# Performance work log

Hardware: AMD Instinct MI355X
Metric: run time of the kernel (lower is better)

The kernel has to match this reference:

```python
import jax, jax.numpy as jnp
import numpy as np

B, C, O = 16, 32, 32
IH, IW = 64, 64
KH, KW = 3, 3
PH, PW = 1, 1
SH, SW = 1, 1
OH = (IH + 2 * PH - KH) // SH + 1  # 64
OW = (IW + 2 * PW - KW) // SW + 1  # 64


def setup_inputs() -> dict:
    key = jax.random.key(0)
    kx, kw = jax.random.split(key)
    x = jax.random.normal(kx, (B, C, IH, IW), dtype=jnp.float32)
    # per-output-location (non-shared) weights: (O, C, OH, OW, KH*KW)
    weight = jax.random.normal(kw, (O, C, OH, OW, KH * KW), dtype=jnp.float32)
    return {"x": x, "weight": weight}


def _patches(x):
    # pad=1 on both spatial dims, then extract KHxKW patches with stride 1
    xp = jnp.pad(x, ((0, 0), (0, 0), (PH, PH), (PW, PW)))
    # ordering matches torch unfold(2,kh).unfold(3,kw) -> flatten last two dims
    pats = [xp[:, :, i : i + OH * SH : SH, j : j + OW * SW : SW]
            for i in range(KH) for j in range(KW)]
    return jnp.stack(pats, axis=-1)  # [B, C, OH, OW, KH*KW]


def reference(x, weight):
    p = _patches(x)  # [B, C, OH, OW, K]
    # fused broadcast-mul + sum over (C, K): per-pixel independent contraction
    out = jnp.einsum('bchwk,ochwk->bohw', p, weight)
    return out  # [B, O, OH, OW]
```

## Files before the change

kernel.cpp:

```cpp
#include <hip/hip_runtime.h>
#include <hip/hip_bf16.h>


#define CIN  32
#define OCH  32
#define HH   64
#define WW   64
#define BB   8
#define OO   2
#define CC   16

typedef float f32x4 __attribute__((ext_vector_type(4), aligned(4)));

__device__ __forceinline__ float lane_pick(int byte_addr, float v) {
    return __int_as_float(__builtin_amdgcn_ds_bpermute(byte_addr, __float_as_int(v)));
}

__global__ __launch_bounds__(256)
void lc2d_kernel(const float* __restrict__ x,
                 const float* __restrict__ wt,
                 float* __restrict__ out) {
    const int w  = threadIdx.x;
    const int h  = blockIdx.x * 4 + threadIdx.y;
    const int og = blockIdx.y;
    const int bz = blockIdx.z & 1;
    const int cg = blockIdx.z >> 1;
    const int o0 = og * OO;
    const int b0 = bz * BB;
    const int c0 = cg * CC;

    const float mt = (h > 0)      ? 1.f : 0.f;
    const float mb = (h < HH - 1) ? 1.f : 0.f;
    const float ml = (w > 0)      ? 1.f : 0.f;
    const float mr = (w < WW - 1) ? 1.f : 0.f;
    const int iht = (h > 0)      ? h - 1 : 0;
    const int ihb = (h < HH - 1) ? h + 1 : HH - 1;

    const int lup = ((w > 0)  ? w - 1 : 0)  << 2;
    const int ldn = ((w < 63) ? w + 1 : 63) << 2;

    float acc[OO * BB];
#pragma unroll
    for (int i = 0; i < OO * BB; ++i) acc[i] = 0.f;

    const size_t WSTRC = (size_t)HH * WW * 9;
    const size_t WSTRO = (size_t)CIN * WSTRC;
    const float* wpa = wt + (size_t)o0 * WSTRO + (size_t)c0 * WSTRC
                          + ((size_t)h * WW + w) * 9;
    const float* wpb = wpa + WSTRO;

    const float* xb0 = x + ((size_t)b0 * CIN + c0) * (HH * WW);
    const int ro_t = iht * WW + w;
    const int ro_m = h   * WW + w;
    const int ro_b = ihb * WW + w;

    f32x4 a03 = *(const f32x4*)(wpa);
    f32x4 a47 = *(const f32x4*)(wpa + 4);
    float a8  = wpa[8];
    f32x4 b03 = *(const f32x4*)(wpb);
    f32x4 b47 = *(const f32x4*)(wpb + 4);
    float b8  = wpb[8];

    for (int c = 0; c < CC; ++c) {
        const float wa0 = a03.x * (mt * ml), wa1 = a03.y * mt, wa2 = a03.z * (mt * mr);
        const float wa3 = a03.w * ml,        wa4 = a47.x,      wa5 = a47.y * mr;
        const float wa6 = a47.z * (mb * ml), wa7 = a47.w * mb, wa8 = a8 * (mb * mr);
        const float wb0 = b03.x * (mt * ml), wb1 = b03.y * mt, wb2 = b03.z * (mt * mr);
        const float wb3 = b03.w * ml,        wb4 = b47.x,      wb5 = b47.y * mr;
        const float wb6 = b47.z * (mb * ml), wb7 = b47.w * mb, wb8 = b8 * (mb * mr);

        const int cn = (c + 1 < CC) ? c + 1 : c;
        const float* npa = wpa + (size_t)cn * WSTRC;
        const float* npb = wpb + (size_t)cn * WSTRC;
        a03 = *(const f32x4*)(npa);
        a47 = *(const f32x4*)(npa + 4);
        a8  = npa[8];
        b03 = *(const f32x4*)(npb);
        b47 = *(const f32x4*)(npb + 4);
        b8  = npb[8];

        const float* xc = xb0 + (size_t)c * (HH * WW);
#pragma unroll
        for (int b = 0; b < BB; ++b) {
            const float* xp = xc + (size_t)b * (CIN * HH * WW);
            const float xt = xp[ro_t];
            const float xm = xp[ro_m];
            const float xd = xp[ro_b];
            const float xtl = lane_pick(lup, xt), xtr = lane_pick(ldn, xt);
            const float xml = lane_pick(lup, xm), xmr = lane_pick(ldn, xm);
            const float xdl = lane_pick(lup, xd), xdr = lane_pick(ldn, xd);

            float a = acc[b];
            a = fmaf(xtl, wa0, a); a = fmaf(xt, wa1, a); a = fmaf(xtr, wa2, a);
            a = fmaf(xml, wa3, a); a = fmaf(xm, wa4, a); a = fmaf(xmr, wa5, a);
            a = fmaf(xdl, wa6, a); a = fmaf(xd, wa7, a); a = fmaf(xdr, wa8, a);
            acc[b] = a;

            float bq = acc[BB + b];
            bq = fmaf(xtl, wb0, bq); bq = fmaf(xt, wb1, bq); bq = fmaf(xtr, wb2, bq);
            bq = fmaf(xml, wb3, bq); bq = fmaf(xm, wb4, bq); bq = fmaf(xmr, wb5, bq);
            bq = fmaf(xdl, wb6, bq); bq = fmaf(xd, wb7, bq); bq = fmaf(xdr, wb8, bq);
            acc[BB + b] = bq;
        }
    }

#pragma unroll
    for (int b = 0; b < BB; ++b) {
#pragma unroll
        for (int oo = 0; oo < OO; ++oo) {
            atomicAdd(out + (((size_t)(b0 + b) * OCH + (o0 + oo)) * HH + h) * WW + w,
                      acc[oo * BB + b]);
        }
    }
}

extern "C" void kernel_launch(void* const* d_in, const int* in_sizes, int n_in,
                              void* d_out, int out_size, void* d_ws, size_t ws_size,
                              hipStream_t stream) {
    const float* x  = (const float*)d_in[0];
    const float* wt = (const float*)d_in[1];
    float* out = (float*)d_out;

    hipMemsetAsync(out, 0, (size_t)out_size * sizeof(float), stream);

    dim3 block(64, 4);
    dim3 grid(HH / 4, OCH / OO, 4);
    lc2d_kernel<<<grid, block, 0, stream>>>(x, wt, out);
}
```

Measured before the change: 59.20 us.

## Double-buffer input rows across channels and pipeline lane permutes ahead of FMAs

Restructures the channel loop into a two-stage software pipeline: the x rows for the next channel are loaded into a second register buffer while the current channel is computed, alongside the existing weight prefetch. The ds_bpermute neighbor fetches are issued two batches ahead of the FMAs that use them, to hide permute latency. Launch bounds now request 4 blocks per CU. The extra buffers raise register pressure, and the launch-bound hint may force spills or cut occupancy.

New measurement: 103.4 us. 74.6% more time.

```diff
diff --git a/kernel.cpp b/kernel.cpp
--- a/kernel.cpp
+++ b/kernel.cpp
@@ -16,16 +16,93 @@
     return __int_as_float(__builtin_amdgcn_ds_bpermute(byte_addr, __float_as_int(v)));
 }
 
-__global__ __launch_bounds__(256)
+#define WSTRC ((size_t)HH * WW * 9)
+#define WSTRO ((size_t)CIN * WSTRC)
+#define XB    ((size_t)CIN * HH * WW)
+
+__device__ __forceinline__ void step(
+    int c, const float* __restrict__ wpa, const float* __restrict__ wpb,
+    const float* __restrict__ xbase,
+    float (&XC)[3][BB], float (&XN)[3][BB],
+    f32x4& cA03, f32x4& cA47, float& cA8,
+    f32x4& cB03, f32x4& cB47, float& cB8,
+    f32x4& nA03, f32x4& nA47, float& nA8,
+    f32x4& nB03, f32x4& nB47, float& nB8,
+    float (&acc)[OO * BB],
+    int ro0, int ro1, int ro2, int lup, int ldn,
+    float mt, float mb, float ml, float mr,
+    float mtml, float mtmr, float mbml, float mbmr)
+{
+    const int cn = (c + 1 < CC) ? c + 1 : c;
+    const float* npa = wpa + (size_t)cn * WSTRC;
+    const float* npb = wpb + (size_t)cn * WSTRC;
+    nA03 = *(const f32x4*)(npa);
+    nA47 = *(const f32x4*)(npa + 4);
+    nA8  = npa[8];
+    nB03 = *(const f32x4*)(npb);
+    nB47 = *(const f32x4*)(npb + 4);
+    nB8  = npb[8];
+
+    const float* xnb = xbase + (size_t)cn * (HH * WW);
+#pragma unroll
+    for (int b = 0; b < BB; ++b) {
+        const float* xp = xnb + (size_t)b * XB;
+        XN[0][b] = xp[ro0]; XN[1][b] = xp[ro1]; XN[2][b] = xp[ro2];
+    }
+
+    const float wa0 = cA03.x * mtml, wa1 = cA03.y * mt, wa2 = cA03.z * mtmr;
+    const float wa3 = cA03.w * ml,   wa4 = cA47.x,      wa5 = cA47.y * mr;
+    const float wa6 = cA47.z * mbml, wa7 = cA47.w * mb, wa8 = cA8 * mbmr;
+    const float wb0 = cB03.x * mtml, wb1 = cB03.y * mt, wb2 = cB03.z * mtmr;
+    const float wb3 = cB03.w * ml,   wb4 = cB47.x,      wb5 = cB47.y * mr;
+    const float wb6 = cB47.z * mbml, wb7 = cB47.w * mb, wb8 = cB8 * mbmr;
+
+    float pr[2][6];
+#pragma unroll
+    for (int b = 0; b < 2; ++b) {
+        pr[b][0] = lane_pick(lup, XC[0][b]); pr[b][1] = lane_pick(ldn, XC[0][b]);
+        pr[b][2] = lane_pick(lup, XC[1][b]); pr[b][3] = lane_pick(ldn, XC[1][b]);
+        pr[b][4] = lane_pick(lup, XC[2][b]); pr[b][5] = lane_pick(ldn, XC[2][b]);
+    }
+#pragma unroll
+    for (int b = 0; b < BB; ++b) {
+        const float xtl = pr[b & 1][0], xtr = pr[b & 1][1];
+        const float xml = pr[b & 1][2], xmr = pr[b & 1][3];
+        const float xdl = pr[b & 1][4], xdr = pr[b & 1][5];
+        const float xt = XC[0][b], xm = XC[1][b], xd = XC[2][b];
+
+        float a = acc[b];
+        a = fmaf(xtl, wa0, a); a = fmaf(xt, wa1, a); a = fmaf(xtr, wa2, a);
+        a = fmaf(xml, wa3, a); a = fmaf(xm, wa4, a); a = fmaf(xmr, wa5, a);
+        a = fmaf(xdl, wa6, a); a = fmaf(xd, wa7, a); a = fmaf(xdr, wa8, a);
+        acc[b] = a;
+
+        float q = acc[BB + b];
+        q = fmaf(xtl, wb0, q); q = fmaf(xt, wb1, q); q = fmaf(xtr, wb2, q);
+        q = fmaf(xml, wb3, q); q = fmaf(xm, wb4, q); q = fmaf(xmr, wb5, q);
+        q = fmaf(xdl, wb6, q); q = fmaf(xd, wb7, q); q = fmaf(xdr, wb8, q);
+        acc[BB + b] = q;
+
+        if (b + 2 < BB) {
+            pr[b & 1][0] = lane_pick(lup, XC[0][b + 2]);
+            pr[b & 1][1] = lane_pick(ldn, XC[0][b + 2]);
+            pr[b & 1][2] = lane_pick(lup, XC[1][b + 2]);
+            pr[b & 1][3] = lane_pick(ldn, XC[1][b + 2]);
+            pr[b & 1][4] = lane_pick(lup, XC[2][b + 2]);
+            pr[b & 1][5] = lane_pick(ldn, XC[2][b + 2]);
+        }
+    }
+}
+
+__global__ __launch_bounds__(256, 4)
 void lc2d_kernel(const float* __restrict__ x,
                  const float* __restrict__ wt,
                  float* __restrict__ out) {
     const int w  = threadIdx.x;
     const int h  = blockIdx.x * 4 + threadIdx.y;
-    const int og = blockIdx.y;
+    const int o0 = blockIdx.y * OO;
     const int bz = blockIdx.z & 1;
     const int cg = blockIdx.z >> 1;
-    const int o0 = og * OO;
     const int b0 = bz * BB;
     const int c0 = cg * CC;
 
@@ -33,75 +110,46 @@
     const float mb = (h < HH - 1) ? 1.f : 0.f;
     const float ml = (w > 0)      ? 1.f : 0.f;
     const float mr = (w < WW - 1) ? 1.f : 0.f;
+    const float mtml = mt * ml, mtmr = mt * mr, mbml = mb * ml, mbmr = mb * mr;
     const int iht = (h > 0)      ? h - 1 : 0;
     const int ihb = (h < HH - 1) ? h + 1 : HH - 1;
-
     const int lup = ((w > 0)  ? w - 1 : 0)  << 2;
     const int ldn = ((w < 63) ? w + 1 : 63) << 2;
+
+    const int ro0 = iht * WW + w, ro1 = h * WW + w, ro2 = ihb * WW + w;
+    const float* xbase = x + ((size_t)b0 * CIN + c0) * (HH * WW);
+
+    const float* wpa = wt + (size_t)o0 * WSTRO + (size_t)c0 * WSTRC
+                          + ((size_t)h * WW + w) * 9;
+    const float* wpb = wpa + WSTRO;
 
     float acc[OO * BB];
 #pragma unroll
     for (int i = 0; i < OO * BB; ++i) acc[i] = 0.f;
 
-    const size_t WSTRC = (size_t)HH * WW * 9;
-    const size_t WSTRO = (size_t)CIN * WSTRC;
-    const float* wpa = wt + (size_t)o0 * WSTRO + (size_t)c0 * WSTRC
-                          + ((size_t)h * WW + w) * 9;
-    const float* wpb = wpa + WSTRO;
+    float X0[3][BB], X1[3][BB];
+    f32x4 A0_03, A0_47, B0_03, B0_47, A1_03, A1_47, B1_03, B1_47;
+    float A0_8, B0_8, A1_8, B1_8;
 
-    const float* xb0 = x + ((size_t)b0 * CIN + c0) * (HH * WW);
-    const int ro_t = iht * WW + w;
-    const int ro_m = h   * WW + w;
-    const int ro_b = ihb * WW + w;
+    A0_03 = *(const f32x4*)(wpa); A0_47 = *(const f32x4*)(wpa + 4); A0_8 = wpa[8];
+    B0_03 = *(const f32x4*)(wpb); B0_47 = *(const f32x4*)(wpb + 4); B0_8 = wpb[8];
+#pragma unroll
+    for (int b = 0; b < BB; ++b) {
+        const float* xp = xbase + (size_t)b * XB;
+        X0[0][b] = xp[ro0]; X0[1][b] = xp[ro1]; X0[2][b] = xp[ro2];
+    }
 
-    f32x4 a03 = *(const f32x4*)(wpa);
-    f32x4 a47 = *(const f32x4*)(wpa + 4);
-    float a8  = wpa[8];
-    f32x4 b03 = *(const f32x4*)(wpb);
-    f32x4 b47 = *(const f32x4*)(wpb + 4);
-    float b8  = wpb[8];
-
-    for (int c = 0; c < CC; ++c) {
-        const float wa0 = a03.x * (mt * ml), wa1 = a03.y * mt, wa2 = a03.z * (mt * mr);
-        const float wa3 = a03.w * ml,        wa4 = a47.x,      wa5 = a47.y * mr;
-        const float wa6 = a47.z * (mb * ml), wa7 = a47.w * mb, wa8 = a8 * (mb * mr);
-        const float wb0 = b03.x * (mt * ml), wb1 = b03.y * mt, wb2 = b03.z * (mt * mr);
-        const float wb3 = b03.w * ml,        wb4 = b47.x,      wb5 = b47.y * mr;
-        const float wb6 = b47.z * (mb * ml), wb7 = b47.w * mb, wb8 = b8 * (mb * mr);
-
-        const int cn = (c + 1 < CC) ? c + 1 : c;
-        const float* npa = wpa + (size_t)cn * WSTRC;
-        const float* npb = wpb + (size_t)cn * WSTRC;
-        a03 = *(const f32x4*)(npa);
-        a47 = *(const f32x4*)(npa + 4);
-        a8  = npa[8];
-        b03 = *(const f32x4*)(npb);
-        b47 = *(const f32x4*)(npb + 4);
-        b8  = npb[8];
-
-        const float* xc = xb0 + (size_t)c * (HH * WW);
-#pragma unroll
-        for (int b = 0; b < BB; ++b) {
-            const float* xp = xc + (size_t)b * (CIN * HH * WW);
-            const float xt = xp[ro_t];
-            const float xm = xp[ro_m];
-            const float xd = xp[ro_b];
-            const float xtl = lane_pick(lup, xt), xtr = lane_pick(ldn, xt);
-            const float xml = lane_pick(lup, xm), xmr = lane_pick(ldn, xm);
-            const float xdl = lane_pick(lup, xd), xdr = lane_pick(ldn, xd);
-
-            float a = acc[b];
-            a = fmaf(xtl, wa0, a); a = fmaf(xt, wa1, a); a = fmaf(xtr, wa2, a);
-            a = fmaf(xml, wa3, a); a = fmaf(xm, wa4, a); a = fmaf(xmr, wa5, a);
-            a = fmaf(xdl, wa6, a); a = fmaf(xd, wa7, a); a = fmaf(xdr, wa8, a);
-            acc[b] = a;
-
-            float bq = acc[BB + b];
-            bq = fmaf(xtl, wb0, bq); bq = fmaf(xt, wb1, bq); bq = fmaf(xtr, wb2, bq);
-            bq = fmaf(xml, wb3, bq); bq = fmaf(xm, wb4, bq); bq = fmaf(xmr, wb5, bq);
-            bq = fmaf(xdl, wb6, bq); bq = fmaf(xd, wb7, bq); bq = fmaf(xdr, wb8, bq);
-            acc[BB + b] = bq;
-        }
+    for (int c = 0; c < CC; c += 2) {
+        step(c,     wpa, wpb, xbase, X0, X1,
+             A0_03, A0_47, A0_8, B0_03, B0_47, B0_8,
+             A1_03, A1_47, A1_8, B1_03, B1_47, B1_8,
+             acc, ro0, ro1, ro2, lup, ldn,
+             mt, mb, ml, mr, mtml, mtmr, mbml, mbmr);
+        step(c + 1, wpa, wpb, xbase, X1, X0,
+             A1_03, A1_47, A1_8, B1_03, B1_47, B1_8,
+             A0_03, A0_47, A0_8, B0_03, B0_47, B0_8,
+             acc, ro0, ro1, ro2, lup, ldn,
+             mt, mb, ml, mr, mtml, mtmr, mbml, mbmr);
     }
 
 #pragma unroll
```
